# Performance work log

Measured on AMD Instinct MI355X. Metric: run time of the kernel, lower is better.

The kernel has to match this reference:

```python
import jax, jax.numpy as jnp
import numpy as np

N, F_IN, H, C, E = 100000, 128, 64, 40, 1600000
NEG_SLOPE = 0.2


def setup_inputs() -> dict:
    key = jax.random.key(0)
    ks = jax.random.split(key, 12)
    s = 0.1
    return {
        "x": jax.random.normal(ks[0], (N, F_IN), jnp.float32),
        "edge_index": jax.random.randint(ks[1], (2, E), 0, N, jnp.int32),
        "W1": jax.random.normal(ks[2], (F_IN, H), jnp.float32) * s,
        "a_src1": jax.random.normal(ks[3], (H,), jnp.float32) * s,
        "a_dst1": jax.random.normal(ks[4], (H,), jnp.float32) * s,
        "b1": jnp.zeros((H,), jnp.float32),
        "W2": jax.random.normal(ks[5], (H, H), jnp.float32) * s,
        "a_src2": jax.random.normal(ks[6], (H,), jnp.float32) * s,
        "a_dst2": jax.random.normal(ks[7], (H,), jnp.float32) * s,
        "b2": jnp.zeros((H,), jnp.float32),
        "Wl": jax.random.normal(ks[8], (H, C), jnp.float32) * s,
        "bl": jnp.zeros((C,), jnp.float32),
    }


def gat_conv(x, src, dst, W, a_src, a_dst, b):
    # PyG GATConv, heads=1, self-loops already appended to (src, dst)
    h = x @ W                                   # [N, H]
    alpha_s = h @ a_src                         # [N]
    alpha_d = h @ a_dst                         # [N]
    e = jax.nn.leaky_relu(alpha_s[src] + alpha_d[dst], NEG_SLOPE)  # [E]
    # segment softmax over incoming edges of each target node
    m = jax.ops.segment_max(e, dst, num_segments=x.shape[0])
    ex = jnp.exp(e - m[dst])
    denom = jax.ops.segment_sum(ex, dst, num_segments=x.shape[0])
    w = ex / (denom[dst] + 1e-16)               # [E]
    out = jax.ops.segment_sum(h[src] * w[:, None], dst, num_segments=x.shape[0])
    return out + b


def reference(x, edge_index, W1, a_src1, a_dst1, b1, W2, a_src2, a_dst2, b2, Wl, bl):
    n = x.shape[0]
    loops = jnp.arange(n, dtype=edge_index.dtype)
    src = jnp.concatenate([edge_index[0], loops])
    dst = jnp.concatenate([edge_index[1], loops])
    h = gat_conv(x, src, dst, W1, a_src1, a_dst1, b1)
    h = jax.nn.relu(h)  # dropout p=0 -> identity
    h = gat_conv(h, src, dst, W2, a_src2, a_dst2, b2)
    logits = h @ Wl + bl
    return jax.nn.log_softmax(logits, axis=-1)
```

## Files before the change

### kernel.cpp

```cpp
#include <hip/hip_runtime.h>
#include <math.h>


#define NEG_SLOPE 0.2f
#define NEG_BIG -3.0e38f

#define BSHIFT 9
#define BSIZE 512
#define BCAP 12288
#define EPB 4096

typedef __bf16 bf16x8 __attribute__((ext_vector_type(8)));
typedef __bf16 bf16x4 __attribute__((ext_vector_type(4)));
typedef float f32x4 __attribute__((ext_vector_type(4)));

__device__ __forceinline__ float lrelu(float x) {
    return x >= 0.f ? x : NEG_SLOPE * x;
}


__global__ __launch_bounds__(256) void fused_scatter_gemm(
        const int* __restrict__ src, const int* __restrict__ dst,
        int* __restrict__ bucketCount, unsigned* __restrict__ ebuf, int E, int SB,
        const float* __restrict__ X, const float* __restrict__ W,
        const float* __restrict__ a_src, const float* __restrict__ a_dst,
        __bf16* __restrict__ Hout, float* __restrict__ as_, float* __restrict__ ad_,
        int N, int nTiles) {
    constexpr int K = 128;
    __shared__ __bf16 Whi[64][K + 8];
    __shared__ __bf16 Wlo[64][K + 8];
    __shared__ int hist[256], base[256], cur[256];

    if (blockIdx.x < (unsigned)SB) {
        const int t = threadIdx.x;
        hist[t] = 0;
        __syncthreads();
        const int e0 = blockIdx.x * EPB;
        const int e1 = min(e0 + EPB, E);
        for (int e = e0 + t; e < e1; e += 256)
            atomicAdd(&hist[dst[e] >> BSHIFT], 1);
        __syncthreads();
        if (hist[t] > 0) base[t] = atomicAdd(&bucketCount[t], hist[t]);
        cur[t] = 0;
        __syncthreads();
        for (int e = e0 + t; e < e1; e += 256) {
            int d = dst[e];
            int b = d >> BSHIFT;
            int r = atomicAdd(&cur[b], 1);
            ebuf[(size_t)b * BCAP + base[b] + r] =
                ((unsigned)src[e] << BSHIFT) | (unsigned)(d & (BSIZE - 1));
        }
        return;
    }

    const int gbid = blockIdx.x - SB;
    for (int idx = threadIdx.x; idx < K * 64; idx += 256) {
        int k = idx >> 6, n = idx & 63;
        float w = W[idx];
        __bf16 hi = (__bf16)w;
        Whi[n][k] = hi;
        Wlo[n][k] = (__bf16)(w - (float)hi);
    }
    __syncthreads();

    const int lane  = threadIdx.x & 63;
    const int wave  = threadIdx.x >> 6;
    const int row16 = lane & 15;
    const int quad  = lane >> 4;

    float asv[4], adv[4];
#pragma unroll
    for (int t = 0; t < 4; ++t) {
        asv[t] = a_src[t * 16 + row16];
        adv[t] = a_dst[t * 16 + row16];
    }

    for (int tile = gbid; tile < nTiles; tile += 1024) {
        const int nbase = tile * 64;
        int gn = nbase + wave * 16 + row16;
        if (gn >= N) gn = N - 1;
        const float* __restrict__ xp = X + (size_t)gn * K + quad * 8;

        float4 xv[K / 16];
#pragma unroll
        for (int c = 0; c < K / 32; ++c) {
            xv[2 * c]     = *(const float4*)(xp + c * 32);
            xv[2 * c + 1] = *(const float4*)(xp + c * 32 + 4);
        }

        f32x4 acc[4] = {{0.f, 0.f, 0.f, 0.f}, {0.f, 0.f, 0.f, 0.f},
                        {0.f, 0.f, 0.f, 0.f}, {0.f, 0.f, 0.f, 0.f}};
#pragma unroll
        for (int kc = 0; kc < K; kc += 32) {
            float xs[8];
            *(float4*)&xs[0] = xv[kc / 16];
            *(float4*)&xs[4] = xv[kc / 16 + 1];
            bf16x8 ahi, alo;
#pragma unroll
            for (int j = 0; j < 8; ++j) {
                __bf16 hi = (__bf16)xs[j];
                ahi[j] = hi;
                alo[j] = (__bf16)(xs[j] - (float)hi);
            }
#pragma unroll
            for (int t = 0; t < 4; ++t) {
                bf16x8 bhi = *(const bf16x8*)&Whi[t * 16 + row16][kc + quad * 8];
                bf16x8 blo = *(const bf16x8*)&Wlo[t * 16 + row16][kc + quad * 8];
                acc[t] = __builtin_amdgcn_mfma_f32_16x16x32_bf16(ahi, bhi, acc[t], 0, 0, 0);
                acc[t] = __builtin_amdgcn_mfma_f32_16x16x32_bf16(ahi, blo, acc[t], 0, 0, 0);
                acc[t] = __builtin_amdgcn_mfma_f32_16x16x32_bf16(alo, bhi, acc[t], 0, 0, 0);
            }
        }

        float ps[4] = {0.f, 0.f, 0.f, 0.f};
        float pd[4] = {0.f, 0.f, 0.f, 0.f};
#pragma unroll
        for (int t = 0; t < 4; ++t) {
#pragma unroll
            for (int r = 0; r < 4; ++r) {
                int gm = nbase + wave * 16 + quad * 4 + r;
                if (gm < N) Hout[(size_t)gm * 64 + t * 16 + row16] = (__bf16)acc[t][r];
                ps[r] = fmaf(acc[t][r], asv[t], ps[r]);
                pd[r] = fmaf(acc[t][r], adv[t], pd[r]);
            }
        }
#pragma unroll
        for (int r = 0; r < 4; ++r) {
#pragma unroll
            for (int d = 1; d < 16; d <<= 1) {
                ps[r] += __shfl_xor(ps[r], d, 64);
                pd[r] += __shfl_xor(pd[r], d, 64);
            }
        }
        if (row16 == 0) {
#pragma unroll
            for (int r = 0; r < 4; ++r) {
                int gm = nbase + wave * 16 + quad * 4 + r;
                if (gm < N) { as_[gm] = ps[r]; ad_[gm] = pd[r]; }
            }
        }
    }
}


__global__ __launch_bounds__(512) void bucket_csr(const unsigned* __restrict__ ebuf,
                                                  const int* __restrict__ bucketCount,
                                                  int* __restrict__ offs,
                                                  int* __restrict__ csr, int N, int E) {
    __shared__ int hist[512], scan[512], bscan[256];
    const int b = blockIdx.x;
    const int t = threadIdx.x;

    if (t < 256) bscan[t] = bucketCount[t];
    __syncthreads();
    for (int d = 1; d < 256; d <<= 1) {
        int x = (t < 256 && t >= d) ? bscan[t - d] : 0;
        __syncthreads();
        if (t < 256) bscan[t] += x;
        __syncthreads();
    }
    const int cnt = bucketCount[b];
    const int gbase = bscan[b] - cnt;
    if (b == 0 && t == 0) offs[N] = E;

    const unsigned* __restrict__ eb = ebuf + (size_t)b * BCAP;
    hist[t] = 0;
    __syncthreads();
    for (int i = t; i < cnt; i += 512)
        atomicAdd(&hist[eb[i] & (BSIZE - 1)], 1);
    __syncthreads();
    int v = hist[t];
    scan[t] = v;
    __syncthreads();
    for (int d = 1; d < 512; d <<= 1) {
        int x = (t >= d) ? scan[t - d] : 0;
        __syncthreads();
        scan[t] += x;
        __syncthreads();
    }
    int excl = scan[t] - v;
    int n = b * BSIZE + t;
    if (n < N) offs[n] = gbase + excl;
    hist[t] = excl;
    __syncthreads();
    for (int i = t; i < cnt; i += 512) {
        unsigned rec = eb[i];
        int pos = atomicAdd(&hist[rec & (BSIZE - 1)], 1);
        csr[gbase + pos] = (int)(rec >> BSHIFT);
    }
}


template <int K>
__global__ __launch_bounds__(256) void gemm_mfma(const float* __restrict__ X,
                                                 const float* __restrict__ W,
                                                 const float* __restrict__ a_src,
                                                 const float* __restrict__ a_dst,
                                                 __bf16* __restrict__ Hout,
                                                 float* __restrict__ as_,
                                                 float* __restrict__ ad_,
                                                 int N, int nTiles) {
    __shared__ __bf16 Whi[64][K + 8];
    __shared__ __bf16 Wlo[64][K + 8];
    for (int idx = threadIdx.x; idx < K * 64; idx += 256) {
        int k = idx >> 6, n = idx & 63;
        float w = W[idx];
        __bf16 hi = (__bf16)w;
        Whi[n][k] = hi;
        Wlo[n][k] = (__bf16)(w - (float)hi);
    }
    __syncthreads();

    const int lane  = threadIdx.x & 63;
    const int wave  = threadIdx.x >> 6;
    const int row16 = lane & 15;
    const int quad  = lane >> 4;

    float asv[4], adv[4];
#pragma unroll
    for (int t = 0; t < 4; ++t) {
        asv[t] = a_src[t * 16 + row16];
        adv[t] = a_dst[t * 16 + row16];
    }

    for (int tile = blockIdx.x; tile < nTiles; tile += gridDim.x) {
        const int nbase = tile * 64;
        int gn = nbase + wave * 16 + row16;
        if (gn >= N) gn = N - 1;
        const float* __restrict__ xp = X + (size_t)gn * K + quad * 8;

        float4 xv[K / 16];
#pragma unroll
        for (int c = 0; c < K / 32; ++c) {
            xv[2 * c]     = *(const float4*)(xp + c * 32);
            xv[2 * c + 1] = *(const float4*)(xp + c * 32 + 4);
        }

        f32x4 acc[4] = {{0.f, 0.f, 0.f, 0.f}, {0.f, 0.f, 0.f, 0.f},
                        {0.f, 0.f, 0.f, 0.f}, {0.f, 0.f, 0.f, 0.f}};
#pragma unroll
        for (int kc = 0; kc < K; kc += 32) {
            float xs[8];
            *(float4*)&xs[0] = xv[kc / 16];
            *(float4*)&xs[4] = xv[kc / 16 + 1];
            bf16x8 ahi, alo;
#pragma unroll
            for (int j = 0; j < 8; ++j) {
                __bf16 hi = (__bf16)xs[j];
                ahi[j] = hi;
                alo[j] = (__bf16)(xs[j] - (float)hi);
            }
#pragma unroll
            for (int t = 0; t < 4; ++t) {
                bf16x8 bhi = *(const bf16x8*)&Whi[t * 16 + row16][kc + quad * 8];
                bf16x8 blo = *(const bf16x8*)&Wlo[t * 16 + row16][kc + quad * 8];
                acc[t] = __builtin_amdgcn_mfma_f32_16x16x32_bf16(ahi, bhi, acc[t], 0, 0, 0);
                acc[t] = __builtin_amdgcn_mfma_f32_16x16x32_bf16(ahi, blo, acc[t], 0, 0, 0);
                acc[t] = __builtin_amdgcn_mfma_f32_16x16x32_bf16(alo, bhi, acc[t], 0, 0, 0);
            }
        }

        float ps[4] = {0.f, 0.f, 0.f, 0.f};
        float pd[4] = {0.f, 0.f, 0.f, 0.f};
#pragma unroll
        for (int t = 0; t < 4; ++t) {
#pragma unroll
            for (int r = 0; r < 4; ++r) {
                int gm = nbase + wave * 16 + quad * 4 + r;
                if (gm < N) Hout[(size_t)gm * 64 + t * 16 + row16] = (__bf16)acc[t][r];
                ps[r] = fmaf(acc[t][r], asv[t], ps[r]);
                pd[r] = fmaf(acc[t][r], adv[t], pd[r]);
            }
        }
#pragma unroll
        for (int r = 0; r < 4; ++r) {
#pragma unroll
            for (int d = 1; d < 16; d <<= 1) {
                ps[r] += __shfl_xor(ps[r], d, 64);
                pd[r] += __shfl_xor(pd[r], d, 64);
            }
        }
        if (row16 == 0) {
#pragma unroll
            for (int r = 0; r < 4; ++r) {
                int gm = nbase + wave * 16 + quad * 4 + r;
                if (gm < N) { as_[gm] = ps[r]; ad_[gm] = pd[r]; }
            }
        }
    }
}


__global__ __launch_bounds__(256) void gat_agg(const __bf16* __restrict__ h,
                                               const float* __restrict__ as_,
                                               const float* __restrict__ ad_,
                                               const float* __restrict__ bias,
                                               const int* __restrict__ offs,
                                               const int* __restrict__ csr,
                                               float* __restrict__ out,
                                               int N, int do_relu) {
    int gtid = blockIdx.x * blockDim.x + threadIdx.x;
    int n = __builtin_amdgcn_readfirstlane(gtid >> 6);
    if (n >= N) return;
    const int lane = threadIdx.x & 63;
    const int g  = lane >> 4;
    const int fl = lane & 15;

    int beg = offs[n], end = offs[n + 1];
    float adn = ad_[n];
    float p_self = __expf(lrelu(as_[n] + adn));

    float den = p_self;
    float ax, ay, az, aw;
    {
        bf16x4 t = *(const bf16x4*)(h + (size_t)n * 64 + fl * 4);
        float m0 = (g == 0) ? p_self : 0.f;
        ax = m0 * (float)t[0];
        ay = m0 * (float)t[1];
        az = m0 * (float)t[2];
        aw = m0 * (float)t[3];
    }

    for (int c0 = beg; c0 < end; c0 += 64) {
        int cnt = end - c0;
        if (cnt > 64) cnt = 64;
        int   s_l = (lane < cnt) ? csr[c0 + lane] : 0;
        float p_l = (lane < cnt) ? __expf(lrelu(as_[s_l] + adn)) : 0.f;
        float csum = p_l;
#pragma unroll
        for (int d = 32; d; d >>= 1) csum += __shfl_xor(csum, d, 64);
        den += csum;

        int rounds = (cnt + 3) >> 2;
        for (int r = 0; r < rounds; r += 4) {
            int j0 = (r + 0) * 4 + g, j1 = (r + 1) * 4 + g;
            int j2 = (r + 2) * 4 + g, j3 = (r + 3) * 4 + g;
            float w0 = __shfl(p_l, j0, 64), w1 = __shfl(p_l, j1, 64);
            float w2 = __shfl(p_l, j2, 64), w3 = __shfl(p_l, j3, 64);
            int s0 = __shfl(s_l, j0, 64), s1 = __shfl(s_l, j1, 64);
            int s2 = __shfl(s_l, j2, 64), s3 = __shfl(s_l, j3, 64);
            bf16x4 h0 = *(const bf16x4*)(h + (size_t)s0 * 64 + fl * 4);
            bf16x4 h1 = *(const bf16x4*)(h + (size_t)s1 * 64 + fl * 4);
            bf16x4 h2 = *(const bf16x4*)(h + (size_t)s2 * 64 + fl * 4);
            bf16x4 h3 = *(const bf16x4*)(h + (size_t)s3 * 64 + fl * 4);
            ax = fmaf(w0, (float)h0[0], ax); ay = fmaf(w0, (float)h0[1], ay);
            az = fmaf(w0, (float)h0[2], az); aw = fmaf(w0, (float)h0[3], aw);
            ax = fmaf(w1, (float)h1[0], ax); ay = fmaf(w1, (float)h1[1], ay);
            az = fmaf(w1, (float)h1[2], az); aw = fmaf(w1, (float)h1[3], aw);
            ax = fmaf(w2, (float)h2[0], ax); ay = fmaf(w2, (float)h2[1], ay);
            az = fmaf(w2, (float)h2[2], az); aw = fmaf(w2, (float)h2[3], aw);
            ax = fmaf(w3, (float)h3[0], ax); ay = fmaf(w3, (float)h3[1], ay);
            az = fmaf(w3, (float)h3[2], az); aw = fmaf(w3, (float)h3[3], aw);
        }
    }

#pragma unroll
    for (int d = 16; d <= 32; d <<= 1) {
        ax += __shfl_xor(ax, d, 64);
        ay += __shfl_xor(ay, d, 64);
        az += __shfl_xor(az, d, 64);
        aw += __shfl_xor(aw, d, 64);
    }
    if (g == 0) {
        float inv = 1.f / (den + 1e-16f);
        const float4 b4 = *(const float4*)(bias + fl * 4);
        float4 o;
        o.x = fmaf(ax, inv, b4.x);
        o.y = fmaf(ay, inv, b4.y);
        o.z = fmaf(az, inv, b4.z);
        o.w = fmaf(aw, inv, b4.w);
        if (do_relu) {
            o.x = fmaxf(o.x, 0.f); o.y = fmaxf(o.y, 0.f);
            o.z = fmaxf(o.z, 0.f); o.w = fmaxf(o.w, 0.f);
        }
        *(float4*)(out + (size_t)n * 64 + fl * 4) = o;
    }
}


__global__ __launch_bounds__(256) void final_lsm(const float* __restrict__ h,
                                                 const float* __restrict__ Wl,
                                                 const float* __restrict__ bl,
                                                 float* __restrict__ out,
                                                 int N, int nTiles) {
    __shared__ __bf16 Whi[48][72];
    __shared__ __bf16 Wlo[48][72];
    __shared__ float bls[48];
    for (int idx = threadIdx.x; idx < 48 * 64; idx += 256) {
        int c = idx >> 6, k = idx & 63;
        float w = (c < 40) ? Wl[k * 40 + c] : 0.f;
        __bf16 hi = (__bf16)w;
        Whi[c][k] = hi;
        Wlo[c][k] = (__bf16)(w - (float)hi);
    }
    if (threadIdx.x < 48) bls[threadIdx.x] = (threadIdx.x < 40) ? bl[threadIdx.x] : 0.f;
    __syncthreads();

    const int lane  = threadIdx.x & 63;
    const int wave  = threadIdx.x >> 6;
    const int col16 = lane & 15;
    const int quad  = lane >> 4;

    for (int tile = blockIdx.x; tile < nTiles; tile += gridDim.x) {
        const int nbase = tile * 64;
        int gn = nbase + wave * 16 + col16;
        if (gn >= N) gn = N - 1;
        const float* __restrict__ xp = h + (size_t)gn * 64 + quad * 8;
        float4 xv[4];
        xv[0] = *(const float4*)(xp);
        xv[1] = *(const float4*)(xp + 4);
        xv[2] = *(const float4*)(xp + 32);
        xv[3] = *(const float4*)(xp + 36);

        f32x4 acc[3] = {{0.f, 0.f, 0.f, 0.f}, {0.f, 0.f, 0.f, 0.f},
                        {0.f, 0.f, 0.f, 0.f}};
#pragma unroll
        for (int kc = 0; kc < 64; kc += 32) {
            float xs[8];
            *(float4*)&xs[0] = xv[kc / 16];
            *(float4*)&xs[4] = xv[kc / 16 + 1];
            bf16x8 ahi, alo;
#pragma unroll
            for (int j = 0; j < 8; ++j) {
                __bf16 hi = (__bf16)xs[j];
                ahi[j] = hi;
                alo[j] = (__bf16)(xs[j] - (float)hi);
            }
#pragma unroll
            for (int t = 0; t < 3; ++t) {
                bf16x8 bhi = *(const bf16x8*)&Whi[t * 16 + col16][kc + quad * 8];
                bf16x8 blo = *(const bf16x8*)&Wlo[t * 16 + col16][kc + quad * 8];
                acc[t] = __builtin_amdgcn_mfma_f32_16x16x32_bf16(ahi, bhi, acc[t], 0, 0, 0);
                acc[t] = __builtin_amdgcn_mfma_f32_16x16x32_bf16(ahi, blo, acc[t], 0, 0, 0);
                acc[t] = __builtin_amdgcn_mfma_f32_16x16x32_bf16(alo, bhi, acc[t], 0, 0, 0);
            }
        }

#pragma unroll
        for (int r = 0; r < 4; ++r) {
            int gm = nbase + wave * 16 + quad * 4 + r;
            float l0 = acc[0][r] + bls[col16];
            float l1 = acc[1][r] + bls[16 + col16];
            float l2 = (col16 < 8) ? (acc[2][r] + bls[32 + col16]) : NEG_BIG;
            float mx = fmaxf(fmaxf(l0, l1), l2);
#pragma unroll
            for (int d = 1; d < 16; d <<= 1) mx = fmaxf(mx, __shfl_xor(mx, d, 64));
            float s = __expf(l0 - mx) + __expf(l1 - mx) +
                      ((col16 < 8) ? __expf(l2 - mx) : 0.f);
#pragma unroll
            for (int d = 1; d < 16; d <<= 1) s += __shfl_xor(s, d, 64);
            float lse = mx + __logf(s);
            if (gm < N) {
                out[(size_t)gm * 40 + col16]      = l0 - lse;
                out[(size_t)gm * 40 + 16 + col16] = l1 - lse;
                if (col16 < 8) out[(size_t)gm * 40 + 32 + col16] = l2 - lse;
            }
        }
    }
}


extern "C" void kernel_launch(void* const* d_in, const int* in_sizes, int n_in,
                              void* d_out, int out_size, void* d_ws, size_t ws_size,
                              hipStream_t stream) {
    const float* x      = (const float*)d_in[0];
    const int*   ei     = (const int*)d_in[1];
    const float* W1     = (const float*)d_in[2];
    const float* a_src1 = (const float*)d_in[3];
    const float* a_dst1 = (const float*)d_in[4];
    const float* b1     = (const float*)d_in[5];
    const float* W2     = (const float*)d_in[6];
    const float* a_src2 = (const float*)d_in[7];
    const float* a_dst2 = (const float*)d_in[8];
    const float* b2     = (const float*)d_in[9];
    const float* Wl     = (const float*)d_in[10];
    const float* bl     = (const float*)d_in[11];

    const int N = in_sizes[0] / 128;
    const int E = in_sizes[1] / 2;
    const int* src = ei;
    const int* dst = ei + E;
    const int nbuck = (N + BSIZE - 1) >> BSHIFT;
    const int SB = (E + EPB - 1) / EPB;

    char* p = (char*)d_ws;
    auto alloc = [&](size_t bytes) -> void* {
        void* r = (void*)p;
        p += (bytes + 255) & ~(size_t)255;
        return r;
    };
    int*      offs        = (int*)alloc((size_t)(N + 1) * 4);
    int*      bucketCount = (int*)alloc(256 * 4);
    unsigned* ebuf        = (unsigned*)alloc((size_t)nbuck * BCAP * 4);
    int*      csr         = (int*)alloc((size_t)E * 4);
    __bf16*   hbf         = (__bf16*)alloc((size_t)N * 64 * 2);
    float*    bufB        = (float*)alloc((size_t)N * 64 * 4);
    float*    as_         = (float*)alloc((size_t)N * 4);
    float*    ad_         = (float*)alloc((size_t)N * 4);

    hipMemsetAsync(bucketCount, 0, 256 * 4, stream);

    const int nTiles = (N + 63) / 64;
    int aggBlocks = (N * 64 + 255) / 256;

    fused_scatter_gemm<<<SB + 1024, 256, 0, stream>>>(
        src, dst, bucketCount, ebuf, E, SB,
        x, W1, a_src1, a_dst1, hbf, as_, ad_, N, nTiles);
    bucket_csr<<<nbuck, 512, 0, stream>>>(ebuf, bucketCount, offs, csr, N, E);
    gat_agg<<<aggBlocks, 256, 0, stream>>>(hbf, as_, ad_, b1, offs, csr, bufB, N, 1);
    gemm_mfma<64><<<1024, 256, 0, stream>>>(bufB, W2, a_src2, a_dst2, hbf, as_, ad_, N, nTiles);
    gat_agg<<<aggBlocks, 256, 0, stream>>>(hbf, as_, ad_, b2, offs, csr, bufB, N, 0);
    final_lsm<<<nTiles, 256, 0, stream>>>(bufB, Wl, bl, (float*)d_out, N, nTiles);
}
```

Measured before the change: 284.8 us.

## Store aggregation outputs in bf16, widen gather lanes, replace block scans with wave scans

The aggregation kernel now writes its output as bf16 instead of fp32. That halves the intermediate activation traffic, and the following GEMM and final log-softmax kernels can load bf16 directly, dropping the hi/lo split of the activations and one of the three MFMAs per tile. The gather loop gives each lane 8 features using 16-byte bf16x8 loads, which means 8 edges per round instead of 4 and one more butterfly step in the reduction. The bucket CSR kernel replaces its shared-memory Hillis-Steele scans with wave shuffle scans and a wave-level sum to get the bucket base. The cost is lower precision in the intermediate activations, which risks accuracy tolerance.

```diff
diff --git a/kernel.cpp b/kernel.cpp
--- a/kernel.cpp
+++ b/kernel.cpp
@@ -16,6 +16,15 @@
 
 __device__ __forceinline__ float lrelu(float x) {
     return x >= 0.f ? x : NEG_SLOPE * x;
+}
+
+__device__ __forceinline__ int wave_incl_scan(int v, int lane) {
+#pragma unroll
+    for (int d = 1; d < 64; d <<= 1) {
+        int t = __shfl_up(v, d, 64);
+        if (lane >= d) v += t;
+    }
+    return v;
 }
 
 
@@ -147,59 +156,58 @@
                                                   const int* __restrict__ bucketCount,
                                                   int* __restrict__ offs,
                                                   int* __restrict__ csr, int N, int E) {
-    __shared__ int hist[512], scan[512], bscan[256];
+    __shared__ int hist[512], cursor[512], wsum[8];
     const int b = blockIdx.x;
     const int t = threadIdx.x;
-
-    if (t < 256) bscan[t] = bucketCount[t];
-    __syncthreads();
-    for (int d = 1; d < 256; d <<= 1) {
-        int x = (t < 256 && t >= d) ? bscan[t - d] : 0;
-        __syncthreads();
-        if (t < 256) bscan[t] += x;
-        __syncthreads();
-    }
+    const int lane = t & 63;
+    const int w = t >> 6;
+
+    int v = (t < 256 && t < b) ? bucketCount[t] : 0;
+#pragma unroll
+    for (int d = 32; d; d >>= 1) v += __shfl_xor(v, d, 64);
+    if (lane == 0) wsum[w] = v;
+    hist[t] = 0;
+    __syncthreads();
+    int gbase = 0;
+#pragma unroll
+    for (int i = 0; i < 8; ++i) gbase += wsum[i];
     const int cnt = bucketCount[b];
-    const int gbase = bscan[b] - cnt;
     if (b == 0 && t == 0) offs[N] = E;
 
     const unsigned* __restrict__ eb = ebuf + (size_t)b * BCAP;
-    hist[t] = 0;
-    __syncthreads();
     for (int i = t; i < cnt; i += 512)
         atomicAdd(&hist[eb[i] & (BSIZE - 1)], 1);
     __syncthreads();
-    int v = hist[t];
-    scan[t] = v;
-    __syncthreads();
-    for (int d = 1; d < 512; d <<= 1) {
-        int x = (t >= d) ? scan[t - d] : 0;
-        __syncthreads();
-        scan[t] += x;
-        __syncthreads();
-    }
-    int excl = scan[t] - v;
+
+    int hv = hist[t];
+    int incl = wave_incl_scan(hv, lane);
+    if (lane == 63) wsum[w] = incl;
+    __syncthreads();
+    int prefix = 0;
+    for (int i = 0; i < 8; ++i) prefix += (i < w) ? wsum[i] : 0;
+    int excl = incl - hv + prefix;
     int n = b * BSIZE + t;
     if (n < N) offs[n] = gbase + excl;
-    hist[t] = excl;
-    __syncthreads();
+    cursor[t] = excl;
+    __syncthreads();
+
     for (int i = t; i < cnt; i += 512) {
         unsigned rec = eb[i];
-        int pos = atomicAdd(&hist[rec & (BSIZE - 1)], 1);
+        int pos = atomicAdd(&cursor[rec & (BSIZE - 1)], 1);
         csr[gbase + pos] = (int)(rec >> BSHIFT);
     }
 }
 
 
-template <int K>
-__global__ __launch_bounds__(256) void gemm_mfma(const float* __restrict__ X,
-                                                 const float* __restrict__ W,
-                                                 const float* __restrict__ a_src,
-                                                 const float* __restrict__ a_dst,
-                                                 __bf16* __restrict__ Hout,
-                                                 float* __restrict__ as_,
-                                                 float* __restrict__ ad_,
-                                                 int N, int nTiles) {
+__global__ __launch_bounds__(256) void gemm_mfma2(const __bf16* __restrict__ X,
+                                                  const float* __restrict__ W,
+                                                  const float* __restrict__ a_src,
+                                                  const float* __restrict__ a_dst,
+                                                  __bf16* __restrict__ Hout,
+                                                  float* __restrict__ as_,
+                                                  float* __restrict__ ad_,
+                                                  int N, int nTiles) {
+    constexpr int K = 64;
     __shared__ __bf16 Whi[64][K + 8];
     __shared__ __bf16 Wlo[64][K + 8];
     for (int idx = threadIdx.x; idx < K * 64; idx += 256) {
@@ -227,36 +235,21 @@
         const int nbase = tile * 64;
         int gn = nbase + wave * 16 + row16;
         if (gn >= N) gn = N - 1;
-        const float* __restrict__ xp = X + (size_t)gn * K + quad * 8;
-
-        float4 xv[K / 16];
-#pragma unroll
-        for (int c = 0; c < K / 32; ++c) {
-            xv[2 * c]     = *(const float4*)(xp + c * 32);
-            xv[2 * c + 1] = *(const float4*)(xp + c * 32 + 4);
-        }
+        const __bf16* __restrict__ xp = X + (size_t)gn * K + quad * 8;
+        bf16x8 a0 = *(const bf16x8*)(xp);
+        bf16x8 a1 = *(const bf16x8*)(xp + 32);
 
         f32x4 acc[4] = {{0.f, 0.f, 0.f, 0.f}, {0.f, 0.f, 0.f, 0.f},
                         {0.f, 0.f, 0.f, 0.f}, {0.f, 0.f, 0.f, 0.f}};
 #pragma unroll
         for (int kc = 0; kc < K; kc += 32) {
-            float xs[8];
-            *(float4*)&xs[0] = xv[kc / 16];
-            *(float4*)&xs[4] = xv[kc / 16 + 1];
-            bf16x8 ahi, alo;
-#pragma unroll
-            for (int j = 0; j < 8; ++j) {
-                __bf16 hi = (__bf16)xs[j];
-                ahi[j] = hi;
-                alo[j] = (__bf16)(xs[j] - (float)hi);
-            }
+            bf16x8 a = (kc == 0) ? a0 : a1;
 #pragma unroll
             for (int t = 0; t < 4; ++t) {
                 bf16x8 bhi = *(const bf16x8*)&Whi[t * 16 + row16][kc + quad * 8];
                 bf16x8 blo = *(const bf16x8*)&Wlo[t * 16 + row16][kc + quad * 8];
-                acc[t] = __builtin_amdgcn_mfma_f32_16x16x32_bf16(ahi, bhi, acc[t], 0, 0, 0);
-                acc[t] = __builtin_amdgcn_mfma_f32_16x16x32_bf16(ahi, blo, acc[t], 0, 0, 0);
-                acc[t] = __builtin_amdgcn_mfma_f32_16x16x32_bf16(alo, bhi, acc[t], 0, 0, 0);
+                acc[t] = __builtin_amdgcn_mfma_f32_16x16x32_bf16(a, bhi, acc[t], 0, 0, 0);
+                acc[t] = __builtin_amdgcn_mfma_f32_16x16x32_bf16(a, blo, acc[t], 0, 0, 0);
             }
         }
 
@@ -297,28 +290,26 @@
                                                const float* __restrict__ bias,
                                                const int* __restrict__ offs,
                                                const int* __restrict__ csr,
-                                               float* __restrict__ out,
+                                               __bf16* __restrict__ out,
                                                int N, int do_relu) {
     int gtid = blockIdx.x * blockDim.x + threadIdx.x;
     int n = __builtin_amdgcn_readfirstlane(gtid >> 6);
     if (n >= N) return;
     const int lane = threadIdx.x & 63;
-    const int g  = lane >> 4;
-    const int fl = lane & 15;
+    const int g  = lane >> 3;
+    const int fl = lane & 7;
 
     int beg = offs[n], end = offs[n + 1];
     float adn = ad_[n];
     float p_self = __expf(lrelu(as_[n] + adn));
 
     float den = p_self;
-    float ax, ay, az, aw;
+    float acc[8];
     {
-        bf16x4 t = *(const bf16x4*)(h + (size_t)n * 64 + fl * 4);
+        bf16x8 t = *(const bf16x8*)(h + (size_t)n * 64 + fl * 8);
         float m0 = (g == 0) ? p_self : 0.f;
-        ax = m0 * (float)t[0];
-        ay = m0 * (float)t[1];
-        az = m0 * (float)t[2];
-        aw = m0 * (float)t[3];
+#pragma unroll
+        for (int i = 0; i < 8; ++i) acc[i] = m0 * (float)t[i];
     }
 
     for (int c0 = beg; c0 < end; c0 += 64) {
@@ -331,54 +322,51 @@
         for (int d = 32; d; d >>= 1) csum += __shfl_xor(csum, d, 64);
         den += csum;
 
-        int rounds = (cnt + 3) >> 2;
+        int rounds = (cnt + 7) >> 3;
         for (int r = 0; r < rounds; r += 4) {
-            int j0 = (r + 0) * 4 + g, j1 = (r + 1) * 4 + g;
-            int j2 = (r + 2) * 4 + g, j3 = (r + 3) * 4 + g;
+            int j0 = (r + 0) * 8 + g, j1 = (r + 1) * 8 + g;
+            int j2 = (r + 2) * 8 + g, j3 = (r + 3) * 8 + g;
             float w0 = __shfl(p_l, j0, 64), w1 = __shfl(p_l, j1, 64);
             float w2 = __shfl(p_l, j2, 64), w3 = __shfl(p_l, j3, 64);
             int s0 = __shfl(s_l, j0, 64), s1 = __shfl(s_l, j1, 64);
             int s2 = __shfl(s_l, j2, 64), s3 = __shfl(s_l, j3, 64);
-            bf16x4 h0 = *(const bf16x4*)(h + (size_t)s0 * 64 + fl * 4);
-            bf16x4 h1 = *(const bf16x4*)(h + (size_t)s1 * 64 + fl * 4);
-            bf16x4 h2 = *(const bf16x4*)(h + (size_t)s2 * 64 + fl * 4);
-            bf16x4 h3 = *(const bf16x4*)(h + (size_t)s3 * 64 + fl * 4);
-            ax = fmaf(w0, (float)h0[0], ax); ay = fmaf(w0, (float)h0[1], ay);
-            az = fmaf(w0, (float)h0[2], az); aw = fmaf(w0, (float)h0[3], aw);
-            ax = fmaf(w1, (float)h1[0], ax); ay = fmaf(w1, (float)h1[1], ay);
-            az = fmaf(w1, (float)h1[2], az); aw = fmaf(w1, (float)h1[3], aw);
-            ax = fmaf(w2, (float)h2[0], ax); ay = fmaf(w2, (float)h2[1], ay);
-            az = fmaf(w2, (float)h2[2], az); aw = fmaf(w2, (float)h2[3], aw);
-            ax = fmaf(w3, (float)h3[0], ax); ay = fmaf(w3, (float)h3[1], ay);
-            az = fmaf(w3, (float)h3[2], az); aw = fmaf(w3, (float)h3[3], aw);
-        }
-    }
-
-#pragma unroll
-    for (int d = 16; d <= 32; d <<= 1) {
-        ax += __shfl_xor(ax, d, 64);
-        ay += __shfl_xor(ay, d, 64);
-        az += __shfl_xor(az, d, 64);
-        aw += __shfl_xor(aw, d, 64);
+            bf16x8 h0 = *(const bf16x8*)(h + (size_t)s0 * 64 + fl * 8);
+            bf16x8 h1 = *(const bf16x8*)(h + (size_t)s1 * 64 + fl * 8);
+            bf16x8 h2 = *(const bf16x8*)(h + (size_t)s2 * 64 + fl * 8);
+            bf16x8 h3 = *(const bf16x8*)(h + (size_t)s3 * 64 + fl * 8);
+#pragma unroll
+            for (int i = 0; i < 8; ++i) {
+                acc[i] = fmaf(w0, (float)h0[i], acc[i]);
+                acc[i] = fmaf(w1, (float)h1[i], acc[i]);
+                acc[i] = fmaf(w2, (float)h2[i], acc[i]);
+                acc[i] = fmaf(w3, (float)h3[i], acc[i]);
+            }
+        }
+    }
+
+#pragma unroll
+    for (int d = 8; d < 64; d <<= 1) {
+#pragma unroll
+        for (int i = 0; i < 8; ++i) acc[i] += __shfl_xor(acc[i], d, 64);
     }
     if (g == 0) {
         float inv = 1.f / (den + 1e-16f);
-        const float4 b4 = *(const float4*)(bias + fl * 4);
-        float4 o;
-        o.x = fmaf(ax, inv, b4.x);
-        o.y = fmaf(ay, inv, b4.y);
-        o.z = fmaf(az, inv, b4.z);
-        o.w = fmaf(aw, inv, b4.w);
-        if (do_relu) {
-            o.x = fmaxf(o.x, 0.f); o.y = fmaxf(o.y, 0.f);
-            o.z = fmaxf(o.z, 0.f); o.w = fmaxf(o.w, 0.f);
-        }
-        *(float4*)(out + (size_t)n * 64 + fl * 4) = o;
-    }
-}
-
-
-__global__ __launch_bounds__(256) void final_lsm(const float* __restrict__ h,
+        float bv[8];
+        *(float4*)&bv[0] = *(const float4*)(bias + fl * 8);
+        *(float4*)&bv[4] = *(const float4*)(bias + fl * 8 + 4);
+        bf16x8 ov;
+#pragma unroll
+        for (int i = 0; i < 8; ++i) {
+            float o = fmaf(acc[i], inv, bv[i]);
+            if (do_relu) o = fmaxf(o, 0.f);
+            ov[i] = (__bf16)o;
+        }
+        *(bf16x8*)(out + (size_t)n * 64 + fl * 8) = ov;
+    }
+}
+
+
+__global__ __launch_bounds__(256) void final_lsm(const __bf16* __restrict__ h,
                                                  const float* __restrict__ Wl,
                                                  const float* __restrict__ bl,
                                                  float* __restrict__ out,
@@ -405,34 +393,21 @@
         const int nbase = tile * 64;
         int gn = nbase + wave * 16 + col16;
         if (gn >= N) gn = N - 1;
-        const float* __restrict__ xp = h + (size_t)gn * 64 + quad * 8;
-        float4 xv[4];
-        xv[0] = *(const float4*)(xp);
-        xv[1] = *(const float4*)(xp + 4);
-        xv[2] = *(const float4*)(xp + 32);
-        xv[3] = *(const float4*)(xp + 36);
+        const __bf16* __restrict__ xp = h + (size_t)gn * 64 + quad * 8;
+        bf16x8 a0 = *(const bf16x8*)(xp);
+        bf16x8 a1 = *(const bf16x8*)(xp + 32);
 
         f32x4 acc[3] = {{0.f, 0.f, 0.f, 0.f}, {0.f, 0.f, 0.f, 0.f},
                         {0.f, 0.f, 0.f, 0.f}};
 #pragma unroll
         for (int kc = 0; kc < 64; kc += 32) {
-            float xs[8];
-            *(float4*)&xs[0] = xv[kc / 16];
-            *(float4*)&xs[4] = xv[kc / 16 + 1];
-            bf16x8 ahi, alo;
-#pragma unroll
-            for (int j = 0; j < 8; ++j) {
-                __bf16 hi = (__bf16)xs[j];
-                ahi[j] = hi;
-                alo[j] = (__bf16)(xs[j] - (float)hi);
-            }
+            bf16x8 a = (kc == 0) ? a0 : a1;
 #pragma unroll
             for (int t = 0; t < 3; ++t) {
                 bf16x8 bhi = *(const bf16x8*)&Whi[t * 16 + col16][kc + quad * 8];
                 bf16x8 blo = *(const bf16x8*)&Wlo[t * 16 + col16][kc + quad * 8];
-                acc[t] = __builtin_amdgcn_mfma_f32_16x16x32_bf16(ahi, bhi, acc[t], 0, 0, 0);
-                acc[t] = __builtin_amdgcn_mfma_f32_16x16x32_bf16(ahi, blo, acc[t], 0, 0, 0);
-                acc[t] = __builtin_amdgcn_mfma_f32_16x16x32_bf16(alo, bhi, acc[t], 0, 0, 0);
+                acc[t] = __builtin_amdgcn_mfma_f32_16x16x32_bf16(a, bhi, acc[t], 0, 0, 0);
+                acc[t] = __builtin_amdgcn_mfma_f32_16x16x32_bf16(a, blo, acc[t], 0, 0, 0);
             }
         }
 
@@ -494,7 +469,7 @@
     unsigned* ebuf        = (unsigned*)alloc((size_t)nbuck * BCAP * 4);
     int*      csr         = (int*)alloc((size_t)E * 4);
     __bf16*   hbf         = (__bf16*)alloc((size_t)N * 64 * 2);
-    float*    bufB        = (float*)alloc((size_t)N * 64 * 4);
+    __bf16*   habg        = (__bf16*)alloc((size_t)N * 64 * 2);
     float*    as_         = (float*)alloc((size_t)N * 4);
     float*    ad_         = (float*)alloc((size_t)N * 4);
 
@@ -507,8 +482,8 @@
         src, dst, bucketCount, ebuf, E, SB,
         x, W1, a_src1, a_dst1, hbf, as_, ad_, N, nTiles);
     bucket_csr<<<nbuck, 512, 0, stream>>>(ebuf, bucketCount, offs, csr, N, E);
-    gat_agg<<<aggBlocks, 256, 0, stream>>>(hbf, as_, ad_, b1, offs, csr, bufB, N, 1);
-    gemm_mfma<64><<<1024, 256, 0, stream>>>(bufB, W2, a_src2, a_dst2, hbf, as_, ad_, N, nTiles);
-    gat_agg<<<aggBlocks, 256, 0, stream>>>(hbf, as_, ad_, b2, offs, csr, bufB, N, 0);
-    final_lsm<<<nTiles, 256, 0, stream>>>(bufB, Wl, bl, (float*)d_out, N, nTiles);
-}
+    gat_agg<<<aggBlocks, 256, 0, stream>>>(hbf, as_, ad_, b1, offs, csr, habg, N, 1);
+    gemm_mfma2<<<1024, 256, 0, stream>>>(habg, W2, a_src2, a_dst2, hbf, as_, ad_, N, nTiles);
+    gat_agg<<<aggBlocks, 256, 0, stream>>>(hbf, as_, ad_, b2, offs, csr, habg, N, 0);
+    final_lsm<<<nTiles, 256, 0, stream>>>(habg, Wl, bl, (float*)d_out, N, nTiles);
+}
```

Measured after the change: 300.7 us. 5.6% more time.
